# Kernel optimization log

Measured on AMD Instinct MI355X. Metric: run time of the kernel, lower is better.

Reference implementation:

```python
import jax, jax.numpy as jnp
import numpy as np

N, E, IN, HID, HEADS, OUT = 20000, 320000, 64, 32, 8, 128
EPS_SM = 1e-16


def setup_inputs() -> dict:
    key = jax.random.key(0)
    ks = iter(jax.random.split(key, 40))
    def g(shape, scale=0.1):
        return jax.random.normal(next(ks), shape, dtype=jnp.float32) * scale
    inp = {
        "x": jax.random.normal(next(ks), (N, IN), dtype=jnp.float32),
        "edge_index": jax.random.randint(next(ks), (2, E), 0, N, dtype=jnp.int64),
        # layer 0: GATConv(64 -> 32, heads=8, concat) => dim 256
        "W0": g((IN, HEADS * HID)), "b0": jnp.zeros((HEADS * HID,), jnp.float32),
        "as0": g((HEADS, HID)), "ad0": g((HEADS, HID)),
        "lng0": jnp.ones((HEADS * HID,), jnp.float32), "lnb0": jnp.zeros((HEADS * HID,), jnp.float32),
        "rW0": g((IN, HEADS * HID)), "rb0": jnp.zeros((HEADS * HID,), jnp.float32),
        "rw0": jnp.ones((1,), jnp.float32),
        # layer 1: GATConv(256 -> 32, heads=8, concat) => dim 256, residual = Identity
        "W1": g((HEADS * HID, HEADS * HID)), "b1": jnp.zeros((HEADS * HID,), jnp.float32),
        "as1": g((HEADS, HID)), "ad1": g((HEADS, HID)),
        "lng1": jnp.ones((HEADS * HID,), jnp.float32), "lnb1": jnp.zeros((HEADS * HID,), jnp.float32),
        "rw1": jnp.ones((1,), jnp.float32),
        # layer 2: GATConv(256 -> 128, heads=8, concat=False mean) => dim 128
        "W2": g((HEADS * HID, HEADS * OUT)), "b2": jnp.zeros((OUT,), jnp.float32),
        "as2": g((HEADS, OUT)), "ad2": g((HEADS, OUT)),
        "lng2": jnp.ones((OUT,), jnp.float32), "lnb2": jnp.zeros((OUT,), jnp.float32),
        "rW2": g((HEADS * HID, OUT)), "rb2": jnp.zeros((OUT,), jnp.float32),
        "rw2": jnp.ones((1,), jnp.float32),
    }
    return inp


def _gat_conv(x, src, dst, W, b, a_s, a_d, heads, out_c, concat):
    n = x.shape[0]
    h = (x @ W).reshape(n, heads, out_c)            # [N,H,C]
    al_s = jnp.sum(h * a_s, axis=-1)                 # [N,H]
    al_d = jnp.sum(h * a_d, axis=-1)
    e = jax.nn.leaky_relu(al_s[src] + al_d[dst], 0.2)  # [E,H]
    m = jax.ops.segment_max(e, dst, num_segments=n)
    m = jnp.where(jnp.isfinite(m), m, 0.0)
    ex = jnp.exp(e - m[dst])
    denom = jax.ops.segment_sum(ex, dst, num_segments=n)
    alpha = ex / (denom[dst] + EPS_SM)               # [E,H]
    msg = alpha[:, :, None] * h[src]                 # [E,H,C]
    out = jax.ops.segment_sum(msg, dst, num_segments=n)  # [N,H,C]
    if concat:
        return out.reshape(n, heads * out_c) + b
    return out.mean(axis=1) + b


def _layer_norm(x, g, b, eps=1e-5):
    mu = x.mean(-1, keepdims=True)
    var = x.var(-1, keepdims=True)
    return (x - mu) * jax.lax.rsqrt(var + eps) * g + b


def reference(x, edge_index, W0, b0, as0, ad0, lng0, lnb0, rW0, rb0, rw0,
              W1, b1, as1, ad1, lng1, lnb1, rw1,
              W2, b2, as2, ad2, lng2, lnb2, rW2, rb2, rw2):
    ei = edge_index.astype(jnp.int32)
    ar = jnp.arange(N, dtype=jnp.int32)
    src = jnp.concatenate([ei[0], ar])               # add self loops
    dst = jnp.concatenate([ei[1], ar])

    # layer 0 (eval mode: dropout is identity)
    g0 = _gat_conv(x, src, dst, W0, b0, as0, ad0, HEADS, HID, True)
    h = _layer_norm(g0, lng0, lnb0) + jax.nn.sigmoid(rw0) * (x @ rW0 + rb0)
    h = jax.nn.elu(h)

    # layer 1 (residual projection = Identity)
    g1 = _gat_conv(h, src, dst, W1, b1, as1, ad1, HEADS, HID, True)
    h = jax.nn.elu(_layer_norm(g1, lng1, lnb1) + jax.nn.sigmoid(rw1) * h)

    # layer 2 (concat=False -> mean over heads)
    g2 = _gat_conv(h, src, dst, W2, b2, as2, ad2, HEADS, OUT, False)
    out = _layer_norm(g2, lng2, lnb2) + jax.nn.sigmoid(rw2) * (h @ rW2 + rb2)
    return out
```

## Files before the change

kernel.cpp:

```cpp
#include <hip/hip_runtime.h>
#include <cstddef>
#include <cstdint>

#define NN 20000
#define EE 320000
#define ET (EE + NN)

typedef __attribute__((ext_vector_type(8))) short bf16x8;
typedef __attribute__((ext_vector_type(4))) float f32x4;

__device__ __forceinline__ unsigned short f2bf_rne(float f) {
  unsigned int u = __float_as_uint(f);
  u += 0x7FFF + ((u >> 16) & 1);
  return (unsigned short)(u >> 16);
}

__device__ __forceinline__ float bf2f(unsigned short b) {
  return __uint_as_float(((unsigned int)b) << 16);
}

__device__ __forceinline__ f32x4 up2(uint2 p) {
  f32x4 v = {__uint_as_float(p.x << 16), __uint_as_float(p.x & 0xFFFF0000u),
             __uint_as_float(p.y << 16), __uint_as_float(p.y & 0xFFFF0000u)};
  return v;
}


__global__ __launch_bounds__(256) void prep_all(
    const float* __restrict__ x, unsigned short* __restrict__ xbf,
    const float* __restrict__ W0, unsigned short* __restrict__ W0T,
    const float* __restrict__ rW0, unsigned short* __restrict__ rW0T,
    const float* __restrict__ W1, unsigned short* __restrict__ W1T,
    const float* __restrict__ rW2, unsigned short* __restrict__ rW2T,
    const float* __restrict__ W2, const float* __restrict__ as2,
    const float* __restrict__ ad2, unsigned short* __restrict__ V16,
    unsigned short* __restrict__ WstkT, int* __restrict__ deg2, int full) {
  int b = blockIdx.x, t = threadIdx.x;
  if (b < 5000) {
    int i = b * 256 + t;
    if (i < NN * 64) xbf[i] = f2bf_rne(x[i]);
    return;
  }
  b -= 5000;
  if (b < 64) {
    int idx = b * 256 + t, n = idx >> 6, k = idx & 63;
    W0T[idx] = f2bf_rne(W0[(size_t)k * 256 + n]);
    return;
  }
  b -= 64;
  if (b < 64) {
    int idx = b * 256 + t, n = idx >> 6, k = idx & 63;
    rW0T[idx] = f2bf_rne(rW0[(size_t)k * 256 + n]);
    return;
  }
  b -= 64;
  if (b < 256) {
    int idx = b * 256 + t, n = idx >> 8, k = idx & 255;
    W1T[idx] = f2bf_rne(W1[(size_t)k * 256 + n]);
    return;
  }
  b -= 256;
  if (b < 128) {
    int idx = b * 256 + t, n = idx >> 8, k = idx & 255;
    rW2T[idx] = f2bf_rne(rW2[(size_t)k * 128 + n]);
    return;
  }
  b -= 128;
  if (b < 157) {
    int i = b * 256 + t;
    if (i < 2 * NN) deg2[i] = 0;
    return;
  }
  b -= 157;
  if (!full) return;
  if (b < 16) {
    int r = b, k = t, h = r & 7;
    const float* av = (r < 8) ? (as2 + h * 128) : (ad2 + h * 128);
    const float* wr = W2 + (size_t)k * 1024 + h * 128;
    float v = 0.f;
#pragma unroll 4
    for (int c = 0; c < 128; ++c) v += wr[c] * av[c];
    V16[(size_t)r * 256 + k] = f2bf_rne(v);
    return;
  }
  b -= 16;
  if (b < 128) {
    int c = b, k = t;
#pragma unroll
    for (int h = 0; h < 8; ++h)
      WstkT[(size_t)c * 2048 + h * 256 + k] =
          f2bf_rne(0.125f * W2[(size_t)k * 1024 + h * 128 + c]);
  }
}

#define PREP_BLOCKS (5000 + 64 + 64 + 256 + 128 + 157 + 16 + 128)


__global__ __launch_bounds__(256) void zero_f32(float* __restrict__ p, int n) {
  int i = blockIdx.x * 256 + threadIdx.x;
  if (i < n) p[i] = 0.f;
}

__global__ void tconv(const float* __restrict__ src, unsigned short* __restrict__ dst,
                      int N) {
  int n = blockIdx.x, k = threadIdx.x, K = blockDim.x;
  dst[(size_t)n * K + k] = f2bf_rne(src[(size_t)k * N + n]);
}


__global__ __launch_bounds__(256) void count_kernel(const int* __restrict__ ei,
                                                    int* __restrict__ deg) {
  int e = blockIdx.x * 256 + threadIdx.x;
  if (e < EE) {
    int d = ei[EE + e];
    if (d >= 0 && d < NN) atomicAdd(&deg[d], 1);
  }
}

__global__ __launch_bounds__(1024) void scan_blk(const int* __restrict__ deg,
    int* __restrict__ offs, int* __restrict__ bsum) {
  __shared__ int s[1024];
  int b = blockIdx.x, tid = threadIdx.x;
  int i = b * 1024 + tid;
  s[tid] = (i < NN) ? (deg[i] + 1) : 0;
  __syncthreads();
  for (int off = 1; off < 1024; off <<= 1) {
    int t = (tid >= off) ? s[tid - off] : 0;
    __syncthreads();
    s[tid] += t;
    __syncthreads();
  }
  if (i < NN) offs[i + 1] = s[tid];
  if (tid == 1023) bsum[b] = s[1023];
}

__global__ __launch_bounds__(256) void scan_add(int* __restrict__ offs,
    const int* __restrict__ bsum) {
  int i = blockIdx.x * 256 + threadIdx.x;
  if (i == 0) offs[0] = 0;
  if (i < NN) {
    int b = i >> 10;
    int pre = 0;
    for (int k = 0; k < b; ++k) pre += bsum[k];
    offs[i + 1] += pre;
  }
}

__global__ __launch_bounds__(256) void scatter_kernel(const int* __restrict__ ei,
    const int* __restrict__ offs, int* __restrict__ cursor, int* __restrict__ csr) {
  int e = blockIdx.x * 256 + threadIdx.x;
  if (e >= ET) return;
  int s, d;
  if (e < EE) { s = ei[e]; d = ei[EE + e]; }
  else        { s = e - EE; d = s; }
  if (s < 0 || s >= NN || d < 0 || d >= NN) return;
  int pos = atomicAdd(&cursor[d], 1);
  csr[offs[d] + pos] = s;
}


__global__ __launch_bounds__(256) void gemm_mfma(const unsigned short* __restrict__ A,
    const unsigned short* __restrict__ BT, const float* __restrict__ bias,
    float* __restrict__ C, int M, int K, int ldc) {
  int bm = blockIdx.y * 64, bn = blockIdx.x * 64;
  int tid = threadIdx.x;
  int w = tid >> 6, l = tid & 63;
  int wm = bm + w * 16;
  if (wm >= M) return;
  int lane16 = l & 15, q = l >> 4;
  const unsigned short* ap = A + (size_t)(wm + lane16) * K + q * 8;
  const unsigned short* bp = BT + (size_t)(bn + lane16) * K + q * 8;
  f32x4 acc0 = {0.f, 0.f, 0.f, 0.f}, acc1 = acc0, acc2 = acc0, acc3 = acc0;
#pragma unroll 2
  for (int k0 = 0; k0 < K; k0 += 32) {
    bf16x8 a  = *(const bf16x8*)(ap + k0);
    bf16x8 b0 = *(const bf16x8*)(bp + k0);
    bf16x8 b1 = *(const bf16x8*)(bp + (size_t)16 * K + k0);
    bf16x8 b2 = *(const bf16x8*)(bp + (size_t)32 * K + k0);
    bf16x8 b3 = *(const bf16x8*)(bp + (size_t)48 * K + k0);
    acc0 = __builtin_amdgcn_mfma_f32_16x16x32_bf16(a, b0, acc0, 0, 0, 0);
    acc1 = __builtin_amdgcn_mfma_f32_16x16x32_bf16(a, b1, acc1, 0, 0, 0);
    acc2 = __builtin_amdgcn_mfma_f32_16x16x32_bf16(a, b2, acc2, 0, 0, 0);
    acc3 = __builtin_amdgcn_mfma_f32_16x16x32_bf16(a, b3, acc3, 0, 0, 0);
  }
  int row0 = wm + q * 4;
  int c0 = bn + lane16;
  float bi0 = bias ? bias[c0]      : 0.f;
  float bi1 = bias ? bias[c0 + 16] : 0.f;
  float bi2 = bias ? bias[c0 + 32] : 0.f;
  float bi3 = bias ? bias[c0 + 48] : 0.f;
#pragma unroll
  for (int r = 0; r < 4; ++r) {
    float* crow = C + (size_t)(row0 + r) * ldc;
    crow[c0]      = acc0[r] + bi0;
    crow[c0 + 16] = acc1[r] + bi1;
    crow[c0 + 32] = acc2[r] + bi2;
    crow[c0 + 48] = acc3[r] + bi3;
  }
}

__global__ __launch_bounds__(256) void gemm_mfma_bf_bias(const unsigned short* __restrict__ A,
    const unsigned short* __restrict__ BT, const float* __restrict__ bias,
    unsigned short* __restrict__ C, int M, int K, int ldc) {
  int bm = blockIdx.y * 64, bn = blockIdx.x * 64;
  int tid = threadIdx.x;
  int w = tid >> 6, l = tid & 63;
  int wm = bm + w * 16;
  if (wm >= M) return;
  int lane16 = l & 15, q = l >> 4;
  const unsigned short* ap = A + (size_t)(wm + lane16) * K + q * 8;
  const unsigned short* bp = BT + (size_t)(bn + lane16) * K + q * 8;
  f32x4 acc0 = {0.f, 0.f, 0.f, 0.f}, acc1 = acc0, acc2 = acc0, acc3 = acc0;
#pragma unroll 2
  for (int k0 = 0; k0 < K; k0 += 32) {
    bf16x8 a  = *(const bf16x8*)(ap + k0);
    bf16x8 b0 = *(const bf16x8*)(bp + k0);
    bf16x8 b1 = *(const bf16x8*)(bp + (size_t)16 * K + k0);
    bf16x8 b2 = *(const bf16x8*)(bp + (size_t)32 * K + k0);
    bf16x8 b3 = *(const bf16x8*)(bp + (size_t)48 * K + k0);
    acc0 = __builtin_amdgcn_mfma_f32_16x16x32_bf16(a, b0, acc0, 0, 0, 0);
    acc1 = __builtin_amdgcn_mfma_f32_16x16x32_bf16(a, b1, acc1, 0, 0, 0);
    acc2 = __builtin_amdgcn_mfma_f32_16x16x32_bf16(a, b2, acc2, 0, 0, 0);
    acc3 = __builtin_amdgcn_mfma_f32_16x16x32_bf16(a, b3, acc3, 0, 0, 0);
  }
  int row0 = wm + q * 4;
  int c0 = bn + lane16;
  float bi0 = bias[c0], bi1 = bias[c0 + 16], bi2 = bias[c0 + 32], bi3 = bias[c0 + 48];
#pragma unroll
  for (int r = 0; r < 4; ++r) {
    unsigned short* crow = C + (size_t)(row0 + r) * ldc;
    crow[c0]      = f2bf_rne(acc0[r] + bi0);
    crow[c0 + 16] = f2bf_rne(acc1[r] + bi1);
    crow[c0 + 32] = f2bf_rne(acc2[r] + bi2);
    crow[c0 + 48] = f2bf_rne(acc3[r] + bi3);
  }
}

__global__ __launch_bounds__(256) void gemm_mfma_bf_al(const unsigned short* __restrict__ A,
    const unsigned short* __restrict__ BT, unsigned short* __restrict__ C,
    const float* __restrict__ as_w, const float* __restrict__ ad_w,
    float* __restrict__ als, float* __restrict__ ald, int M, int K) {
  int bm = blockIdx.y * 64, bn = blockIdx.x * 64;
  int tid = threadIdx.x;
  int w = tid >> 6, l = tid & 63;
  int wm = bm + w * 16;
  if (wm >= M) return;
  int lane16 = l & 15, q = l >> 4;
  const unsigned short* ap = A + (size_t)(wm + lane16) * K + q * 8;
  const unsigned short* bp = BT + (size_t)(bn + lane16) * K + q * 8;
  f32x4 acc0 = {0.f, 0.f, 0.f, 0.f}, acc1 = acc0, acc2 = acc0, acc3 = acc0;
#pragma unroll 2
  for (int k0 = 0; k0 < K; k0 += 32) {
    bf16x8 a  = *(const bf16x8*)(ap + k0);
    bf16x8 b0 = *(const bf16x8*)(bp + k0);
    bf16x8 b1 = *(const bf16x8*)(bp + (size_t)16 * K + k0);
    bf16x8 b2 = *(const bf16x8*)(bp + (size_t)32 * K + k0);
    bf16x8 b3 = *(const bf16x8*)(bp + (size_t)48 * K + k0);
    acc0 = __builtin_amdgcn_mfma_f32_16x16x32_bf16(a, b0, acc0, 0, 0, 0);
    acc1 = __builtin_amdgcn_mfma_f32_16x16x32_bf16(a, b1, acc1, 0, 0, 0);
    acc2 = __builtin_amdgcn_mfma_f32_16x16x32_bf16(a, b2, acc2, 0, 0, 0);
    acc3 = __builtin_amdgcn_mfma_f32_16x16x32_bf16(a, b3, acc3, 0, 0, 0);
  }
  int row0 = wm + q * 4;
  int c0 = bn + lane16;
#pragma unroll
  for (int r = 0; r < 4; ++r) {
    unsigned short* crow = C + (size_t)(row0 + r) * 256;
    crow[c0]      = f2bf_rne(acc0[r]);
    crow[c0 + 16] = f2bf_rne(acc1[r]);
    crow[c0 + 32] = f2bf_rne(acc2[r]);
    crow[c0 + 48] = f2bf_rne(acc3[r]);
  }
  float asA0 = as_w[c0],      asA1 = as_w[c0 + 16];
  float adA0 = ad_w[c0],      adA1 = ad_w[c0 + 16];
  float asB0 = as_w[c0 + 32], asB1 = as_w[c0 + 48];
  float adB0 = ad_w[c0 + 32], adB1 = ad_w[c0 + 48];
  int hA = (bn >> 5), hB = hA + 1;
#pragma unroll
  for (int r = 0; r < 4; ++r) {
    float sA = acc0[r] * asA0 + acc1[r] * asA1;
    float dA = acc0[r] * adA0 + acc1[r] * adA1;
    float sB = acc2[r] * asB0 + acc3[r] * asB1;
    float dB = acc2[r] * adB0 + acc3[r] * adB1;
#pragma unroll
    for (int off = 8; off >= 1; off >>= 1) {
      sA += __shfl_xor(sA, off);
      dA += __shfl_xor(dA, off);
      sB += __shfl_xor(sB, off);
      dB += __shfl_xor(dB, off);
    }
    if (lane16 == 0) {
      int row = row0 + r;
      als[row * 8 + hA] = sA;
      ald[row * 8 + hA] = dA;
      als[row * 8 + hB] = sB;
      ald[row * 8 + hB] = dB;
    }
  }
}

__global__ __launch_bounds__(256) void gemm_al16(const unsigned short* __restrict__ A,
    const unsigned short* __restrict__ V16, float* __restrict__ als,
    float* __restrict__ ald, int M) {
  int bm = blockIdx.x * 64;
  int tid = threadIdx.x;
  int w = tid >> 6, l = tid & 63;
  int wm = bm + w * 16;
  if (wm >= M) return;
  int lane16 = l & 15, q = l >> 4;
  const unsigned short* ap = A + (size_t)(wm + lane16) * 256 + q * 8;
  const unsigned short* bp = V16 + (size_t)lane16 * 256 + q * 8;
  f32x4 acc = {0.f, 0.f, 0.f, 0.f};
#pragma unroll
  for (int k0 = 0; k0 < 256; k0 += 32) {
    bf16x8 a = *(const bf16x8*)(ap + k0);
    bf16x8 b = *(const bf16x8*)(bp + k0);
    acc = __builtin_amdgcn_mfma_f32_16x16x32_bf16(a, b, acc, 0, 0, 0);
  }
  int row0 = wm + q * 4;
  float* dst = (lane16 < 8) ? als : ald;
  int h = lane16 & 7;
#pragma unroll
  for (int r = 0; r < 4; ++r)
    dst[(size_t)(row0 + r) * 8 + h] = acc[r];
}


__global__ __launch_bounds__(256) void gemm_y_tiled(const unsigned short* __restrict__ A,
    const unsigned short* __restrict__ BT, float* __restrict__ P, int M) {
  __shared__ unsigned short sA[64][72];
  __shared__ unsigned short sB[128][72];
  int bm = blockIdx.x * 64, s = blockIdx.y;
  int tid = threadIdx.x;
  int w = tid >> 6, l = tid & 63;
  int lane16 = l & 15, q = l >> 4;
  int soff = s * 512;
  int r = tid >> 3, c = (tid & 7) * 8;
  int rA0 = min(bm + r, M - 1);
  int rA1 = min(bm + r + 32, M - 1);
  f32x4 acc[8] = {};
#pragma unroll 1
  for (int kt = 0; kt < 8; ++kt) {
    int kb = soff + kt * 64 + c;
    *(bf16x8*)&sA[r][c]      = *(const bf16x8*)(A + (size_t)rA0 * 2048 + kb);
    *(bf16x8*)&sA[r + 32][c] = *(const bf16x8*)(A + (size_t)rA1 * 2048 + kb);
#pragma unroll
    for (int rr = 0; rr < 4; ++rr)
      *(bf16x8*)&sB[r + rr * 32][c] = *(const bf16x8*)(BT + (size_t)(r + rr * 32) * 2048 + kb);
    __syncthreads();
#pragma unroll
    for (int kk = 0; kk < 2; ++kk) {
      bf16x8 a = *(const bf16x8*)&sA[w * 16 + lane16][kk * 32 + q * 8];
#pragma unroll
      for (int t = 0; t < 8; ++t) {
        bf16x8 b = *(const bf16x8*)&sB[t * 16 + lane16][kk * 32 + q * 8];
        acc[t] = __builtin_amdgcn_mfma_f32_16x16x32_bf16(a, b, acc[t], 0, 0, 0);
      }
    }
    __syncthreads();
  }
  int row0 = bm + w * 16 + q * 4;
  float* pbase = P + (size_t)s * ((size_t)M * 128);
#pragma unroll
  for (int r2 = 0; r2 < 4; ++r2) {
    if (row0 + r2 < M) {
      float* prow = pbase + (size_t)(row0 + r2) * 128 + lane16;
#pragma unroll
      for (int t = 0; t < 8; ++t) prow[t * 16] = acc[t][r2];
    }
  }
}


__global__ __launch_bounds__(256) void al2(const float* __restrict__ h,
    const float* __restrict__ aw_s, const float* __restrict__ aw_d,
    float* __restrict__ als, float* __restrict__ ald) {
  int n = blockIdx.x, tid = threadIdx.x;
  int j = tid & 127;
  __shared__ float ss[256], sd[256];
  float v = h[(size_t)n * 256 + tid];
  ss[tid] = v * aw_s[tid];
  sd[tid] = v * aw_d[tid];
  __syncthreads();
  for (int off = 64; off > 0; off >>= 1) {
    if (j < off) { ss[tid] += ss[tid + off]; sd[tid] += sd[tid + off]; }
    __syncthreads();
  }
  if (j == 0) {
    int hh = tid >> 7;
    als[n * 2 + hh] = ss[tid];
    ald[n * 2 + hh] = sd[tid];
  }
}


__global__ __launch_bounds__(256) void agg_epi_w(const unsigned short* __restrict__ hG,
    const float* __restrict__ als, const float* __restrict__ ald,
    const int* __restrict__ offs, const int* __restrict__ csr,
    const float* __restrict__ bias, const float* __restrict__ lng,
    const float* __restrict__ lnb, const unsigned short* __restrict__ resb,
    const float* __restrict__ rw, unsigned short* __restrict__ outbf) {
  int w = threadIdx.x >> 6, l = threadIdx.x & 63;
  int n = blockIdx.x * 4 + w;
  if (n >= NN) return;
  int r0 = offs[n], r1 = offs[n + 1], deg = r1 - r0;
  int h8 = l & 7, e8 = l >> 3, hl = l >> 3;
  float aldn = ald[n * 8 + h8];
  f32x4 acc = {0.f, 0.f, 0.f, 0.f};
  float denacc = 0.f;
  for (int c0 = 0; c0 < deg; c0 += 8) {
    int cn = min(8, deg - c0);
    int src_my = csr[r0 + c0 + min(e8, cn - 1)];
    float ev = als[src_my * 8 + h8] + aldn;
    ev = ev >= 0.f ? ev : 0.2f * ev;
    float aexp = (e8 < cn) ? __expf(ev) : 0.f;
    denacc += aexp;
#pragma unroll 2
    for (int e = 0; e < cn; ++e) {
      int s = __shfl(src_my, e * 8);
      float a = __shfl(aexp, e * 8 + hl);
      uint2 p = *(const uint2*)(hG + (size_t)s * 256 + l * 4);
      acc += a * up2(p);
    }
  }
  denacc += __shfl_xor(denacc, 8);
  denacc += __shfl_xor(denacc, 16);
  denacc += __shfl_xor(denacc, 32);
  float den = __shfl(denacc, hl);
  float dinv = 1.f / (den + 1e-16f);
  float4 bi = ((const float4*)bias)[l];
  uint2 pb = ((const uint2*)resb)[(size_t)n * 64 + l];
  f32x4 rr = up2(pb);
  f32x4 val = {acc.x * dinv + bi.x, acc.y * dinv + bi.y,
               acc.z * dinv + bi.z, acc.w * dinv + bi.w};
  float v1 = val.x + val.y + val.z + val.w;
  float v2 = val.x * val.x + val.y * val.y + val.z * val.z + val.w * val.w;
#pragma unroll
  for (int off = 32; off >= 1; off >>= 1) {
    v1 += __shfl_xor(v1, off);
    v2 += __shfl_xor(v2, off);
  }
  float mu = v1 * (1.f / 256.f);
  float var = v2 * (1.f / 256.f) - mu * mu;
  float rs = rsqrtf(var + 1e-5f);
  float sig = 1.f / (1.f + __expf(-rw[0]));
  float4 lg = ((const float4*)lng)[l];
  float4 lb = ((const float4*)lnb)[l];
  float ov[4];
  const float* valp = (const float*)&val;
  const float* rrp = (const float*)&rr;
  const float* lgp = &lg.x;
  const float* lbp = &lb.x;
#pragma unroll
  for (int k = 0; k < 4; ++k) {
    float rv = (valp[k] - mu) * rs * lgp[k] + lbp[k] + sig * rrp[k];
    ov[k] = rv > 0.f ? rv : (__expf(rv) - 1.f);
  }
  uint2 pk;
  pk.x = (unsigned)f2bf_rne(ov[0]) | ((unsigned)f2bf_rne(ov[1]) << 16);
  pk.y = (unsigned)f2bf_rne(ov[2]) | ((unsigned)f2bf_rne(ov[3]) << 16);
  ((uint2*)outbf)[(size_t)n * 64 + l] = pk;
}


__global__ __launch_bounds__(256) void agg_y_w(const unsigned short* __restrict__ hbf,
    const float* __restrict__ als, const float* __restrict__ ald,
    const int* __restrict__ offs, const int* __restrict__ csr,
    unsigned short* __restrict__ Y) {
  int w = threadIdx.x >> 6, l = threadIdx.x & 63;
  int n = blockIdx.x * 4 + w;
  if (n >= NN) return;
  int r0 = offs[n], r1 = offs[n + 1], deg = r1 - r0;
  int h8 = l & 7, e8 = l >> 3;
  float aldn = ald[n * 8 + h8];
  f32x4 accv[8] = {};
  float denacc = 0.f;
  for (int c0 = 0; c0 < deg; c0 += 8) {
    int cn = min(8, deg - c0);
    int src_my = csr[r0 + c0 + min(e8, cn - 1)];
    float ev = als[src_my * 8 + h8] + aldn;
    ev = ev >= 0.f ? ev : 0.2f * ev;
    float aexp = (e8 < cn) ? __expf(ev) : 0.f;
    denacc += aexp;
    for (int e = 0; e < cn; ++e) {
      int s = __shfl(src_my, e * 8);
      uint2 p = *(const uint2*)(hbf + (size_t)s * 256 + l * 4);
      f32x4 v = up2(p);
#pragma unroll
      for (int h = 0; h < 8; ++h) {
        float a = __shfl(aexp, e * 8 + h);
        accv[h] += a * v;
      }
    }
  }
  denacc += __shfl_xor(denacc, 8);
  denacc += __shfl_xor(denacc, 16);
  denacc += __shfl_xor(denacc, 32);
  unsigned short* yrow = Y + (size_t)n * 2048;
#pragma unroll
  for (int h = 0; h < 8; ++h) {
    float dh = __shfl(denacc, h);
    float sc = 1.f / (dh + 1e-16f);
    f32x4 t = accv[h];
    uint2 pk;
    pk.x = (unsigned)f2bf_rne(t.x * sc) | ((unsigned)f2bf_rne(t.y * sc) << 16);
    pk.y = (unsigned)f2bf_rne(t.z * sc) | ((unsigned)f2bf_rne(t.w * sc) << 16);
    *(uint2*)(yrow + h * 256 + l * 4) = pk;
  }
}


__global__ __launch_bounds__(256) void agg2_pair(const float* __restrict__ h2,
    const float* __restrict__ als, const float* __restrict__ ald,
    const int* __restrict__ offs, const int* __restrict__ csr,
    float* __restrict__ acc_out) {
  int n = blockIdx.x, tid = threadIdx.x;
  int r0 = offs[n], r1 = offs[n + 1];
  __shared__ float s_red[256];
  __shared__ float s_dn[2];
  int hh = tid >> 7, j = tid & 127;
  float aldn = ald[n * 2 + hh];
  float sm = 0.f;
  for (int i = r0 + j; i < r1; i += 128) {
    int s = csr[i];
    float ev = als[s * 2 + hh] + aldn;
    ev = ev >= 0.f ? ev : 0.2f * ev;
    sm += __expf(ev);
  }
  s_red[tid] = sm;
  __syncthreads();
  for (int off = 64; off > 0; off >>= 1) {
    if (j < off) s_red[tid] += s_red[tid + off];
    __syncthreads();
  }
  if (j == 0) s_dn[hh] = s_red[tid] + 1e-16f;
  __syncthreads();
  float dinv = 1.f / s_dn[hh];
  float acc = 0.f;
  for (int i = r0; i < r1; ++i) {
    int s = csr[i];
    float ev = als[s * 2 + hh] + aldn;
    ev = ev >= 0.f ? ev : 0.2f * ev;
    float alpha = __expf(ev) * dinv;
    acc += alpha * h2[(size_t)s * 256 + tid];
  }
  s_red[tid] = acc;
  __syncthreads();
  if (tid < 128)
    acc_out[(size_t)n * 128 + tid] += 0.125f * (s_red[tid] + s_red[tid + 128]);
}


__global__ __launch_bounds__(128) void epi_out_res4(const float* __restrict__ P,
    const float* __restrict__ b2, const float* __restrict__ lng,
    const float* __restrict__ lnb, const float* __restrict__ res2,
    const float* __restrict__ rw, float* __restrict__ out) {
  int n = blockIdx.x, tid = threadIdx.x;
  __shared__ float sw1[2], sw2[2];
  size_t stride = (size_t)NN * 128;
  size_t idx = (size_t)n * 128 + tid;
  float g = P[idx] + P[stride + idx] + P[2 * stride + idx] + P[3 * stride + idx] + b2[tid];
  float v1 = g, v2 = g * g;
#pragma unroll
  for (int off = 32; off >= 1; off >>= 1) {
    v1 += __shfl_xor(v1, off);
    v2 += __shfl_xor(v2, off);
  }
  if ((tid & 63) == 0) { sw1[tid >> 6] = v1; sw2[tid >> 6] = v2; }
  __syncthreads();
  float tot1 = sw1[0] + sw1[1], tot2 = sw2[0] + sw2[1];
  float mu = tot1 * (1.f / 128.f);
  float var = tot2 * (1.f / 128.f) - mu * mu;
  float rs = rsqrtf(var + 1e-5f);
  float sig = 1.f / (1.f + __expf(-rw[0]));
  out[idx] = (g - mu) * rs * lng[tid] + lnb[tid] + sig * res2[idx];
}

__global__ __launch_bounds__(128) void epi_out_res(float* __restrict__ acc,
    const float* __restrict__ b2, const float* __restrict__ lng,
    const float* __restrict__ lnb, const float* __restrict__ res2,
    const float* __restrict__ rw) {
  int n = blockIdx.x, tid = threadIdx.x;
  __shared__ float s1[128], s2[128];
  __shared__ float s_mu, s_rs;
  float g = acc[(size_t)n * 128 + tid] + b2[tid];
  s1[tid] = g; s2[tid] = g * g;
  __syncthreads();
  for (int off = 64; off > 0; off >>= 1) {
    if (tid < off) { s1[tid] += s1[tid + off]; s2[tid] += s2[tid + off]; }
    __syncthreads();
  }
  if (tid == 0) {
    float mu = s1[0] * (1.f / 128.f);
    float var = s2[0] * (1.f / 128.f) - mu * mu;
    s_mu = mu; s_rs = rsqrtf(var + 1e-5f);
  }
  __syncthreads();
  float sig = 1.f / (1.f + __expf(-rw[0]));
  float lnv = (g - s_mu) * s_rs * lng[tid] + lnb[tid];
  acc[(size_t)n * 128 + tid] = lnv + sig * res2[(size_t)n * 128 + tid];
}

__global__ __launch_bounds__(128) void epi_out_mv(float* __restrict__ acc,
    const float* __restrict__ b2, const float* __restrict__ lng,
    const float* __restrict__ lnb, const unsigned short* __restrict__ hB,
    const float* __restrict__ rW2, const float* __restrict__ rb2,
    const float* __restrict__ rw) {
  int n = blockIdx.x, tid = threadIdx.x;
  __shared__ float srow[256];
  __shared__ float s1[128], s2[128];
  __shared__ float s_mu, s_rs;
  srow[tid] = bf2f(hB[(size_t)n * 256 + tid]);
  srow[tid + 128] = bf2f(hB[(size_t)n * 256 + tid + 128]);
  float g = acc[(size_t)n * 128 + tid] + b2[tid];
  s1[tid] = g; s2[tid] = g * g;
  __syncthreads();
  for (int off = 64; off > 0; off >>= 1) {
    if (tid < off) { s1[tid] += s1[tid + off]; s2[tid] += s2[tid + off]; }
    __syncthreads();
  }
  if (tid == 0) {
    float mu = s1[0] * (1.f / 128.f);
    float var = s2[0] * (1.f / 128.f) - mu * mu;
    s_mu = mu; s_rs = rsqrtf(var + 1e-5f);
  }
  __syncthreads();
  float rv = rb2[tid];
#pragma unroll 4
  for (int k = 0; k < 256; ++k) rv += srow[k] * rW2[(size_t)k * 128 + tid];
  float sig = 1.f / (1.f + __expf(-rw[0]));
  float lnv = (g - s_mu) * s_rs * lng[tid] + lnb[tid];
  acc[(size_t)n * 128 + tid] = lnv + sig * rv;
}


extern "C" void kernel_launch(void* const* d_in, const int* in_sizes, int n_in,
                              void* d_out, int out_size, void* d_ws, size_t ws_size,
                              hipStream_t stream) {
  const float* x   = (const float*)d_in[0];
  const int*   ei  = (const int*)d_in[1];
  const float* W0  = (const float*)d_in[2];
  const float* b0  = (const float*)d_in[3];
  const float* as0 = (const float*)d_in[4];
  const float* ad0 = (const float*)d_in[5];
  const float* lng0= (const float*)d_in[6];
  const float* lnb0= (const float*)d_in[7];
  const float* rW0 = (const float*)d_in[8];
  const float* rb0 = (const float*)d_in[9];
  const float* rw0 = (const float*)d_in[10];
  const float* W1  = (const float*)d_in[11];
  const float* b1  = (const float*)d_in[12];
  const float* as1 = (const float*)d_in[13];
  const float* ad1 = (const float*)d_in[14];
  const float* lng1= (const float*)d_in[15];
  const float* lnb1= (const float*)d_in[16];
  const float* rw1 = (const float*)d_in[17];
  const float* W2  = (const float*)d_in[18];
  const float* b2  = (const float*)d_in[19];
  const float* as2 = (const float*)d_in[20];
  const float* ad2 = (const float*)d_in[21];
  const float* lng2= (const float*)d_in[22];
  const float* lnb2= (const float*)d_in[23];
  const float* rW2 = (const float*)d_in[24];
  const float* rb2 = (const float*)d_in[25];
  const float* rw2 = (const float*)d_in[26];
  float* outp = (float*)d_out;

  char* w = (char*)d_ws;
  auto carve = [&](size_t bytes) -> char* {
    char* p = w;
    w += (bytes + 255) & ~(size_t)255;
    return p;
  };
  float* bufH = (float*)carve((size_t)NN * 256 * 4);
  float* bufR = (float*)carve((size_t)NN * 256 * 4);
  float* als  = (float*)carve((size_t)NN * 8 * 4);
  float* ald  = (float*)carve((size_t)NN * 8 * 4);
  int* deg    = (int*)carve((size_t)2 * NN * 4);
  int* cursor = deg + NN;
  int* offs   = (int*)carve((size_t)(NN + 1) * 4);
  int* bsum   = (int*)carve((size_t)32 * 4);
  int* csr    = (int*)carve((size_t)ET * 4);
  unsigned short* xbf  = (unsigned short*)carve((size_t)NN * 64 * 2);
  unsigned short* hbf0 = (unsigned short*)carve((size_t)NN * 256 * 2);
  unsigned short* hbf1 = (unsigned short*)carve((size_t)NN * 256 * 2);
  unsigned short* W0T  = (unsigned short*)carve((size_t)256 * 64 * 2);
  unsigned short* rW0T = (unsigned short*)carve((size_t)256 * 64 * 2);
  unsigned short* W1T  = (unsigned short*)carve((size_t)256 * 256 * 2);
  unsigned short* W2T  = (unsigned short*)carve((size_t)1024 * 256 * 2);
  unsigned short* rW2T = (unsigned short*)carve((size_t)128 * 256 * 2);
  size_t base = (size_t)(w - (char*)d_ws);
  if (ws_size < base) return;
  unsigned short* hG = (unsigned short*)bufH;

  size_t full_extra = (((size_t)16 * 256 * 2 + 255) & ~(size_t)255)
                    + (((size_t)128 * 2048 * 2 + 255) & ~(size_t)255)
                    + (((size_t)NN * 2048 * 2 + 255) & ~(size_t)255);
  size_t res2_extra = (((size_t)NN * 128 * 4 + 255) & ~(size_t)255);
  bool full = (ws_size - base) >= full_extra;
  unsigned short *V16 = nullptr, *WstkT = nullptr, *Ybuf = nullptr;
  if (full) {
    V16   = (unsigned short*)carve((size_t)16 * 256 * 2);
    WstkT = (unsigned short*)carve((size_t)128 * 2048 * 2);
    Ybuf  = (unsigned short*)carve((size_t)NN * 2048 * 2);
  }
  float* res2 = nullptr;
  if ((ws_size - (size_t)(w - (char*)d_ws)) >= res2_extra)
    res2 = (float*)carve((size_t)NN * 128 * 4);

  prep_all<<<PREP_BLOCKS, 256, 0, stream>>>(x, xbf, W0, W0T, rW0, rW0T, W1, W1T,
                                            rW2, rW2T, W2, as2, ad2, V16, WstkT,
                                            deg, full ? 1 : 0);
  if (!full) tconv<<<1024, 256, 0, stream>>>(W2, W2T, 1024);

  count_kernel<<<(EE + 255) / 256, 256, 0, stream>>>(ei, deg);
  int nb = (NN + 1023) / 1024;
  scan_blk<<<nb, 1024, 0, stream>>>(deg, offs, bsum);
  scan_add<<<(NN + 255) / 256, 256, 0, stream>>>(offs, bsum);
  scatter_kernel<<<(ET + 255) / 256, 256, 0, stream>>>(ei, offs, cursor, csr);

  dim3 g256(4, (NN + 63) / 64);
  dim3 g128(2, (NN + 63) / 64);
  int gagg = (NN + 3) / 4;

  gemm_mfma_bf_al<<<g256, 256, 0, stream>>>(xbf, W0T, hG, as0, ad0, als, ald, NN, 64);
  gemm_mfma_bf_bias<<<g256, 256, 0, stream>>>(xbf, rW0T, rb0, hbf1, NN, 64, 256);
  agg_epi_w<<<gagg, 256, 0, stream>>>(hG, als, ald, offs, csr, b0, lng0, lnb0,
                                      hbf1, rw0, hbf0);

  gemm_mfma_bf_al<<<g256, 256, 0, stream>>>(hbf0, W1T, hG, as1, ad1, als, ald, NN, 256);
  agg_epi_w<<<gagg, 256, 0, stream>>>(hG, als, ald, offs, csr, b1, lng1, lnb1,
                                      hbf0, rw1, hbf1);

  if (res2)
    gemm_mfma<<<g128, 256, 0, stream>>>(hbf1, rW2T, rb2, res2, NN, 256, 128);
  if (full) {
    gemm_al16<<<(NN + 63) / 64, 256, 0, stream>>>(hbf1, V16, als, ald, NN);
    agg_y_w<<<gagg, 256, 0, stream>>>(hbf1, als, ald, offs, csr, Ybuf);
    if (res2) {
      float* partial = bufH;
      gemm_y_tiled<<<dim3((NN + 63) / 64, 4), 256, 0, stream>>>(Ybuf, WstkT,
                                                                partial, NN);
      epi_out_res4<<<NN, 128, 0, stream>>>(partial, b2, lng2, lnb2, res2, rw2, outp);
    } else {
      gemm_mfma<<<g128, 256, 0, stream>>>(Ybuf, WstkT, nullptr, outp, NN, 2048, 128);
      epi_out_mv<<<NN, 128, 0, stream>>>(outp, b2, lng2, lnb2, hbf1, rW2, rb2, rw2);
    }
  } else {
    zero_f32<<<(NN * 128 + 255) / 256, 256, 0, stream>>>(outp, NN * 128);
    for (int p = 0; p < 4; ++p) {
      gemm_mfma<<<g256, 256, 0, stream>>>(hbf1, W2T + (size_t)p * 256 * 256, nullptr,
                                          bufH, NN, 256, 256);
      al2<<<NN, 256, 0, stream>>>(bufH, as2 + p * 256, ad2 + p * 256, als, ald);
      agg2_pair<<<NN, 256, 0, stream>>>(bufH, als, ald, offs, csr, outp);
    }
    if (res2)
      epi_out_res<<<NN, 128, 0, stream>>>(outp, b2, lng2, lnb2, res2, rw2);
    else
      epi_out_mv<<<NN, 128, 0, stream>>>(outp, b2, lng2, lnb2, hbf1, rW2, rb2, rw2);
  }
}
```

Before: 399.8 us.

## Sort nodes by degree for aggregation and fuse layer GEMM launches

Builds a degree-bucketed node permutation (histogram in scan_blk, bucket prefix, perm_build) so the aggregation kernels process nodes in descending-degree order, which should balance wavefront work across blocks. Merges the layer-0 attention GEMM and residual GEMM into one launch using a z grid dimension, and merges the layer-2 attention-logit GEMM with the residual projection GEMM into one launch. This adds a few small preprocessing kernels and an extra indirection load per node in the aggregation kernels.

```diff
diff --git a/kernel.cpp b/kernel.cpp
--- a/kernel.cpp
+++ b/kernel.cpp
@@ -34,7 +34,7 @@
     const float* __restrict__ rW2, unsigned short* __restrict__ rW2T,
     const float* __restrict__ W2, const float* __restrict__ as2,
     const float* __restrict__ ad2, unsigned short* __restrict__ V16,
-    unsigned short* __restrict__ WstkT, int* __restrict__ deg2, int full) {
+    unsigned short* __restrict__ WstkT, int* __restrict__ zbuf, int full) {
   int b = blockIdx.x, t = threadIdx.x;
   if (b < 5000) {
     int i = b * 256 + t;
@@ -68,7 +68,7 @@
   b -= 128;
   if (b < 157) {
     int i = b * 256 + t;
-    if (i < 2 * NN) deg2[i] = 0;
+    if (i < 2 * NN + 192) zbuf[i] = 0;
     return;
   }
   b -= 157;
@@ -118,12 +118,16 @@
 }
 
 __global__ __launch_bounds__(1024) void scan_blk(const int* __restrict__ deg,
-    int* __restrict__ offs, int* __restrict__ bsum) {
+    int* __restrict__ offs, int* __restrict__ bsum, int* __restrict__ hist) {
   __shared__ int s[1024];
+  __shared__ int lh[64];
   int b = blockIdx.x, tid = threadIdx.x;
+  if (tid < 64) lh[tid] = 0;
   int i = b * 1024 + tid;
-  s[tid] = (i < NN) ? (deg[i] + 1) : 0;
-  __syncthreads();
+  int d = (i < NN) ? (deg[i] + 1) : 0;
+  s[tid] = d;
+  __syncthreads();
+  if (i < NN) atomicAdd(&lh[63 - min(d, 63)], 1);
   for (int off = 1; off < 1024; off <<= 1) {
     int t = (tid >= off) ? s[tid - off] : 0;
     __syncthreads();
@@ -132,6 +136,14 @@
   }
   if (i < NN) offs[i + 1] = s[tid];
   if (tid == 1023) bsum[b] = s[1023];
+  if (tid < 64 && lh[tid]) atomicAdd(&hist[tid], lh[tid]);
+}
+
+__global__ void bucket_prefix(const int* __restrict__ hist, int* __restrict__ boff) {
+  if (threadIdx.x == 0) {
+    int run = 0;
+    for (int k = 0; k < 64; ++k) { boff[k] = run; run += hist[k]; }
+  }
 }
 
 __global__ __launch_bounds__(256) void scan_add(int* __restrict__ offs,
@@ -143,6 +155,17 @@
     int pre = 0;
     for (int k = 0; k < b; ++k) pre += bsum[k];
     offs[i + 1] += pre;
+  }
+}
+
+__global__ __launch_bounds__(256) void perm_build(const int* __restrict__ offs,
+    const int* __restrict__ boff, int* __restrict__ bcur, int* __restrict__ perm) {
+  int n = blockIdx.x * 256 + threadIdx.x;
+  if (n < NN) {
+    int d = offs[n + 1] - offs[n];
+    int key = 63 - min(d, 63);
+    int pos = atomicAdd(&bcur[key], 1);
+    perm[boff[key] + pos] = n;
   }
 }
 
@@ -199,25 +222,30 @@
   }
 }
 
-__global__ __launch_bounds__(256) void gemm_mfma_bf_bias(const unsigned short* __restrict__ A,
-    const unsigned short* __restrict__ BT, const float* __restrict__ bias,
-    unsigned short* __restrict__ C, int M, int K, int ldc) {
+__global__ __launch_bounds__(256) void gemm_l0(const unsigned short* __restrict__ A,
+    const unsigned short* __restrict__ W0T, const unsigned short* __restrict__ rW0T,
+    const float* __restrict__ rb0, unsigned short* __restrict__ hG,
+    unsigned short* __restrict__ resout, const float* __restrict__ as_w,
+    const float* __restrict__ ad_w, float* __restrict__ als,
+    float* __restrict__ ald, int M) {
+  int z = blockIdx.z;
   int bm = blockIdx.y * 64, bn = blockIdx.x * 64;
   int tid = threadIdx.x;
   int w = tid >> 6, l = tid & 63;
   int wm = bm + w * 16;
   if (wm >= M) return;
   int lane16 = l & 15, q = l >> 4;
-  const unsigned short* ap = A + (size_t)(wm + lane16) * K + q * 8;
-  const unsigned short* bp = BT + (size_t)(bn + lane16) * K + q * 8;
+  const unsigned short* BT = z ? rW0T : W0T;
+  const unsigned short* ap = A + (size_t)(wm + lane16) * 64 + q * 8;
+  const unsigned short* bp = BT + (size_t)(bn + lane16) * 64 + q * 8;
   f32x4 acc0 = {0.f, 0.f, 0.f, 0.f}, acc1 = acc0, acc2 = acc0, acc3 = acc0;
-#pragma unroll 2
-  for (int k0 = 0; k0 < K; k0 += 32) {
+#pragma unroll
+  for (int k0 = 0; k0 < 64; k0 += 32) {
     bf16x8 a  = *(const bf16x8*)(ap + k0);
     bf16x8 b0 = *(const bf16x8*)(bp + k0);
-    bf16x8 b1 = *(const bf16x8*)(bp + (size_t)16 * K + k0);
-    bf16x8 b2 = *(const bf16x8*)(bp + (size_t)32 * K + k0);
-    bf16x8 b3 = *(const bf16x8*)(bp + (size_t)48 * K + k0);
+    bf16x8 b1 = *(const bf16x8*)(bp + (size_t)16 * 64 + k0);
+    bf16x8 b2 = *(const bf16x8*)(bp + (size_t)32 * 64 + k0);
+    bf16x8 b3 = *(const bf16x8*)(bp + (size_t)48 * 64 + k0);
     acc0 = __builtin_amdgcn_mfma_f32_16x16x32_bf16(a, b0, acc0, 0, 0, 0);
     acc1 = __builtin_amdgcn_mfma_f32_16x16x32_bf16(a, b1, acc1, 0, 0, 0);
     acc2 = __builtin_amdgcn_mfma_f32_16x16x32_bf16(a, b2, acc2, 0, 0, 0);
@@ -225,14 +253,51 @@
   }
   int row0 = wm + q * 4;
   int c0 = bn + lane16;
-  float bi0 = bias[c0], bi1 = bias[c0 + 16], bi2 = bias[c0 + 32], bi3 = bias[c0 + 48];
+  if (z == 1) {
+    float bi0 = rb0[c0], bi1 = rb0[c0 + 16], bi2 = rb0[c0 + 32], bi3 = rb0[c0 + 48];
+#pragma unroll
+    for (int r = 0; r < 4; ++r) {
+      unsigned short* crow = resout + (size_t)(row0 + r) * 256;
+      crow[c0]      = f2bf_rne(acc0[r] + bi0);
+      crow[c0 + 16] = f2bf_rne(acc1[r] + bi1);
+      crow[c0 + 32] = f2bf_rne(acc2[r] + bi2);
+      crow[c0 + 48] = f2bf_rne(acc3[r] + bi3);
+    }
+    return;
+  }
 #pragma unroll
   for (int r = 0; r < 4; ++r) {
-    unsigned short* crow = C + (size_t)(row0 + r) * ldc;
-    crow[c0]      = f2bf_rne(acc0[r] + bi0);
-    crow[c0 + 16] = f2bf_rne(acc1[r] + bi1);
-    crow[c0 + 32] = f2bf_rne(acc2[r] + bi2);
-    crow[c0 + 48] = f2bf_rne(acc3[r] + bi3);
+    unsigned short* crow = hG + (size_t)(row0 + r) * 256;
+    crow[c0]      = f2bf_rne(acc0[r]);
+    crow[c0 + 16] = f2bf_rne(acc1[r]);
+    crow[c0 + 32] = f2bf_rne(acc2[r]);
+    crow[c0 + 48] = f2bf_rne(acc3[r]);
+  }
+  float asA0 = as_w[c0],      asA1 = as_w[c0 + 16];
+  float adA0 = ad_w[c0],      adA1 = ad_w[c0 + 16];
+  float asB0 = as_w[c0 + 32], asB1 = as_w[c0 + 48];
+  float adB0 = ad_w[c0 + 32], adB1 = ad_w[c0 + 48];
+  int hA = (bn >> 5), hB = hA + 1;
+#pragma unroll
+  for (int r = 0; r < 4; ++r) {
+    float sA = acc0[r] * asA0 + acc1[r] * asA1;
+    float dA = acc0[r] * adA0 + acc1[r] * adA1;
+    float sB = acc2[r] * asB0 + acc3[r] * asB1;
+    float dB = acc2[r] * adB0 + acc3[r] * adB1;
+#pragma unroll
+    for (int off = 8; off >= 1; off >>= 1) {
+      sA += __shfl_xor(sA, off);
+      dA += __shfl_xor(dA, off);
+      sB += __shfl_xor(sB, off);
+      dB += __shfl_xor(dB, off);
+    }
+    if (lane16 == 0) {
+      int row = row0 + r;
+      als[row * 8 + hA] = sA;
+      ald[row * 8 + hA] = dA;
+      als[row * 8 + hB] = sB;
+      ald[row * 8 + hB] = dB;
+    }
   }
 }
 
@@ -299,6 +364,63 @@
   }
 }
 
+__global__ __launch_bounds__(256) void gemm_l2a(const unsigned short* __restrict__ A,
+    const unsigned short* __restrict__ V16, const unsigned short* __restrict__ rW2T,
+    const float* __restrict__ rb2, float* __restrict__ als, float* __restrict__ ald,
+    float* __restrict__ res2, int M) {
+  int bx = blockIdx.x;
+  int bm = blockIdx.y * 64;
+  int tid = threadIdx.x;
+  int w = tid >> 6, l = tid & 63;
+  int wm = bm + w * 16;
+  if (wm >= M) return;
+  int lane16 = l & 15, q = l >> 4;
+  const unsigned short* ap = A + (size_t)(wm + lane16) * 256 + q * 8;
+  if (bx == 0) {
+    const unsigned short* bp = V16 + (size_t)lane16 * 256 + q * 8;
+    f32x4 acc = {0.f, 0.f, 0.f, 0.f};
+#pragma unroll
+    for (int k0 = 0; k0 < 256; k0 += 32) {
+      bf16x8 a = *(const bf16x8*)(ap + k0);
+      bf16x8 b = *(const bf16x8*)(bp + k0);
+      acc = __builtin_amdgcn_mfma_f32_16x16x32_bf16(a, b, acc, 0, 0, 0);
+    }
+    int row0 = wm + q * 4;
+    float* dst = (lane16 < 8) ? als : ald;
+    int h = lane16 & 7;
+#pragma unroll
+    for (int r = 0; r < 4; ++r)
+      dst[(size_t)(row0 + r) * 8 + h] = acc[r];
+    return;
+  }
+  int bn = (bx - 1) * 64;
+  const unsigned short* bp = rW2T + (size_t)(bn + lane16) * 256 + q * 8;
+  f32x4 acc0 = {0.f, 0.f, 0.f, 0.f}, acc1 = acc0, acc2 = acc0, acc3 = acc0;
+#pragma unroll 2
+  for (int k0 = 0; k0 < 256; k0 += 32) {
+    bf16x8 a  = *(const bf16x8*)(ap + k0);
+    bf16x8 b0 = *(const bf16x8*)(bp + k0);
+    bf16x8 b1 = *(const bf16x8*)(bp + (size_t)16 * 256 + k0);
+    bf16x8 b2 = *(const bf16x8*)(bp + (size_t)32 * 256 + k0);
+    bf16x8 b3 = *(const bf16x8*)(bp + (size_t)48 * 256 + k0);
+    acc0 = __builtin_amdgcn_mfma_f32_16x16x32_bf16(a, b0, acc0, 0, 0, 0);
+    acc1 = __builtin_amdgcn_mfma_f32_16x16x32_bf16(a, b1, acc1, 0, 0, 0);
+    acc2 = __builtin_amdgcn_mfma_f32_16x16x32_bf16(a, b2, acc2, 0, 0, 0);
+    acc3 = __builtin_amdgcn_mfma_f32_16x16x32_bf16(a, b3, acc3, 0, 0, 0);
+  }
+  int row0 = wm + q * 4;
+  int c0 = bn + lane16;
+  float bi0 = rb2[c0], bi1 = rb2[c0 + 16], bi2 = rb2[c0 + 32], bi3 = rb2[c0 + 48];
+#pragma unroll
+  for (int r = 0; r < 4; ++r) {
+    float* crow = res2 + (size_t)(row0 + r) * 128;
+    crow[c0]      = acc0[r] + bi0;
+    crow[c0 + 16] = acc1[r] + bi1;
+    crow[c0 + 32] = acc2[r] + bi2;
+    crow[c0 + 48] = acc3[r] + bi3;
+  }
+}
+
 __global__ __launch_bounds__(256) void gemm_al16(const unsigned short* __restrict__ A,
     const unsigned short* __restrict__ V16, float* __restrict__ als,
     float* __restrict__ ald, int M) {
@@ -397,12 +519,14 @@
 __global__ __launch_bounds__(256) void agg_epi_w(const unsigned short* __restrict__ hG,
     const float* __restrict__ als, const float* __restrict__ ald,
     const int* __restrict__ offs, const int* __restrict__ csr,
+    const int* __restrict__ perm,
     const float* __restrict__ bias, const float* __restrict__ lng,
     const float* __restrict__ lnb, const unsigned short* __restrict__ resb,
     const float* __restrict__ rw, unsigned short* __restrict__ outbf) {
   int w = threadIdx.x >> 6, l = threadIdx.x & 63;
-  int n = blockIdx.x * 4 + w;
-  if (n >= NN) return;
+  int idx = blockIdx.x * 4 + w;
+  if (idx >= NN) return;
+  int n = perm[idx];
   int r0 = offs[n], r1 = offs[n + 1], deg = r1 - r0;
   int h8 = l & 7, e8 = l >> 3, hl = l >> 3;
   float aldn = ald[n * 8 + h8];
@@ -466,10 +590,11 @@
 __global__ __launch_bounds__(256) void agg_y_w(const unsigned short* __restrict__ hbf,
     const float* __restrict__ als, const float* __restrict__ ald,
     const int* __restrict__ offs, const int* __restrict__ csr,
-    unsigned short* __restrict__ Y) {
+    const int* __restrict__ perm, unsigned short* __restrict__ Y) {
   int w = threadIdx.x >> 6, l = threadIdx.x & 63;
-  int n = blockIdx.x * 4 + w;
-  if (n >= NN) return;
+  int idx = blockIdx.x * 4 + w;
+  if (idx >= NN) return;
+  int n = perm[idx];
   int r0 = offs[n], r1 = offs[n + 1], deg = r1 - r0;
   int h8 = l & 7, e8 = l >> 3;
   float aldn = ald[n * 8 + h8];
@@ -676,8 +801,12 @@
   float* bufR = (float*)carve((size_t)NN * 256 * 4);
   float* als  = (float*)carve((size_t)NN * 8 * 4);
   float* ald  = (float*)carve((size_t)NN * 8 * 4);
-  int* deg    = (int*)carve((size_t)2 * NN * 4);
+  int* deg    = (int*)carve((size_t)(2 * NN + 192) * 4);
   int* cursor = deg + NN;
+  int* hist   = deg + 2 * NN;
+  int* boff   = hist + 64;
+  int* bcur   = boff + 64;
+  int* perm   = (int*)carve((size_t)NN * 4);
   int* offs   = (int*)carve((size_t)(NN + 1) * 4);
   int* bsum   = (int*)carve((size_t)32 * 4);
   int* csr    = (int*)carve((size_t)ET * 4);
@@ -715,38 +844,41 @@
 
   count_kernel<<<(EE + 255) / 256, 256, 0, stream>>>(ei, deg);
   int nb = (NN + 1023) / 1024;
-  scan_blk<<<nb, 1024, 0, stream>>>(deg, offs, bsum);
+  scan_blk<<<nb, 1024, 0, stream>>>(deg, offs, bsum, hist);
+  bucket_prefix<<<1, 64, 0, stream>>>(hist, boff);
   scan_add<<<(NN + 255) / 256, 256, 0, stream>>>(offs, bsum);
+  perm_build<<<(NN + 255) / 256, 256, 0, stream>>>(offs, boff, bcur, perm);
   scatter_kernel<<<(ET + 255) / 256, 256, 0, stream>>>(ei, offs, cursor, csr);
 
   dim3 g256(4, (NN + 63) / 64);
   dim3 g128(2, (NN + 63) / 64);
   int gagg = (NN + 3) / 4;
 
-  gemm_mfma_bf_al<<<g256, 256, 0, stream>>>(xbf, W0T, hG, as0, ad0, als, ald, NN, 64);
-  gemm_mfma_bf_bias<<<g256, 256, 0, stream>>>(xbf, rW0T, rb0, hbf1, NN, 64, 256);
-  agg_epi_w<<<gagg, 256, 0, stream>>>(hG, als, ald, offs, csr, b0, lng0, lnb0,
-                                      hbf1, rw0, hbf0);
+  gemm_l0<<<dim3(4, (NN + 63) / 64, 2), 256, 0, stream>>>(
+      xbf, W0T, rW0T, rb0, hG, hbf1, as0, ad0, als, ald, NN);
+  agg_epi_w<<<gagg, 256, 0, stream>>>(hG, als, ald, offs, csr, perm, b0, lng0,
+                                      lnb0, hbf1, rw0, hbf0);
 
   gemm_mfma_bf_al<<<g256, 256, 0, stream>>>(hbf0, W1T, hG, as1, ad1, als, ald, NN, 256);
-  agg_epi_w<<<gagg, 256, 0, stream>>>(hG, als, ald, offs, csr, b1, lng1, lnb1,
-                                      hbf0, rw1, hbf1);
-
-  if (res2)
-    gemm_mfma<<<g128, 256, 0, stream>>>(hbf1, rW2T, rb2, res2, NN, 256, 128);
-  if (full) {
+  agg_epi_w<<<gagg, 256, 0, stream>>>(hG, als, ald, offs, csr, perm, b1, lng1,
+                                      lnb1, hbf0, rw1, hbf1);
+
+  if (full && res2) {
+    gemm_l2a<<<dim3(3, (NN + 63) / 64), 256, 0, stream>>>(hbf1, V16, rW2T, rb2,
+                                                          als, ald, res2, NN);
+    agg_y_w<<<gagg, 256, 0, stream>>>(hbf1, als, ald, offs, csr, perm, Ybuf);
+    float* partial = bufH;
+    gemm_y_tiled<<<dim3((NN + 63) / 64, 4), 256, 0, stream>>>(Ybuf, WstkT,
+                                                              partial, NN);
+    epi_out_res4<<<NN, 128, 0, stream>>>(partial, b2, lng2, lnb2, res2, rw2, outp);
+  } else if (full) {
     gemm_al16<<<(NN + 63) / 64, 256, 0, stream>>>(hbf1, V16, als, ald, NN);
-    agg_y_w<<<gagg, 256, 0, stream>>>(hbf1, als, ald, offs, csr, Ybuf);
-    if (res2) {
-      float* partial = bufH;
-      gemm_y_tiled<<<dim3((NN + 63) / 64, 4), 256, 0, stream>>>(Ybuf, WstkT,
-                                                                partial, NN);
-      epi_out_res4<<<NN, 128, 0, stream>>>(partial, b2, lng2, lnb2, res2, rw2, outp);
-    } else {
-      gemm_mfma<<<g128, 256, 0, stream>>>(Ybuf, WstkT, nullptr, outp, NN, 2048, 128);
-      epi_out_mv<<<NN, 128, 0, stream>>>(outp, b2, lng2, lnb2, hbf1, rW2, rb2, rw2);
-    }
+    agg_y_w<<<gagg, 256, 0, stream>>>(hbf1, als, ald, offs, csr, perm, Ybuf);
+    gemm_mfma<<<g128, 256, 0, stream>>>(Ybuf, WstkT, nullptr, outp, NN, 2048, 128);
+    epi_out_mv<<<NN, 128, 0, stream>>>(outp, b2, lng2, lnb2, hbf1, rW2, rb2, rw2);
   } else {
+    if (res2)
+      gemm_mfma<<<g128, 256, 0, stream>>>(hbf1, rW2T, rb2, res2, NN, 256, 128);
     zero_f32<<<(NN * 128 + 255) / 256, 256, 0, stream>>>(outp, NN * 128);
     for (int p = 0; p < 4; ++p) {
       gemm_mfma<<<g256, 256, 0, stream>>>(hbf1, W2T + (size_t)p * 256 * 256, nullptr,
```

New measurement: 438.5 us. 1.1x slower.
